# Optimization experiments

Measured on AMD Instinct MI355X. Metric: run time of the kernel, lower is better.

Reference implementation:

```python
import jax, jax.numpy as jnp
import numpy as np
import math

D_MODEL = 256
N_HEADS = 8
HEAD_DIM = D_MODEL // N_HEADS  # 32
N_LEVELS = 4
N_POINTS = 4
SHAPES = [(112, 112), (56, 56), (28, 28), (14, 14)]
LEN_IN = sum(h * w for h, w in SHAPES)  # 16660
BATCH = 1
LEN_Q = LEN_IN


def _grid_init_bias():
    # Faithful to MSDeformAttn._reset_parameters: directional grid init for sampling_offsets bias.
    thetas = np.arange(N_HEADS, dtype=np.float32) * (2.0 * math.pi / N_HEADS)
    grid = np.stack([np.cos(thetas), np.sin(thetas)], -1)
    grid = grid / np.abs(grid).max(-1, keepdims=True)
    grid = np.tile(grid[:, None, None, :], (1, N_LEVELS, N_POINTS, 1)).copy()
    for i in range(N_POINTS):
        grid[:, :, i, :] *= i + 1
    return jnp.asarray(grid.reshape(-1), dtype=jnp.float32)


def setup_inputs() -> dict:
    key = jax.random.key(0)
    ks = jax.random.split(key, 10)
    s = 1.0 / math.sqrt(D_MODEL)
    return {
        "query": jax.random.normal(ks[0], (BATCH, LEN_Q, D_MODEL), jnp.float32),
        "reference_points": jax.random.uniform(ks[1], (BATCH, LEN_Q, N_LEVELS, 2), jnp.float32),
        "input_flatten": jax.random.normal(ks[2], (BATCH, LEN_IN, D_MODEL), jnp.float32),
        "spatial_shapes": jnp.asarray(SHAPES, dtype=jnp.int32),
        "level_start_index": jnp.asarray(np.cumsum([0] + [h * w for h, w in SHAPES])[:-1], dtype=jnp.int32),
        "W_q": jax.random.normal(ks[3], (D_MODEL, D_MODEL), jnp.float32) * s,
        "b_q": jnp.zeros((D_MODEL,), jnp.float32),
        "W_k": jax.random.normal(ks[4], (D_MODEL, D_MODEL), jnp.float32) * s,
        "b_k": jnp.zeros((D_MODEL,), jnp.float32),
        "W_v": jax.random.normal(ks[5], (D_MODEL, D_MODEL), jnp.float32) * s,
        "b_v": jnp.zeros((D_MODEL,), jnp.float32),
        "W_o": jax.random.normal(ks[6], (D_MODEL, D_MODEL), jnp.float32) * s,
        "b_o": jnp.zeros((D_MODEL,), jnp.float32),
        "W_off": jax.random.normal(ks[7], (D_MODEL, N_HEADS * N_LEVELS * N_POINTS * 2), jnp.float32) * 0.01,
        "b_off": _grid_init_bias(),
    }


def _bilinear_sample(img, grid, H, W):
    # img: (B, H*W, D) flattened feature map; grid: (B, Q, P, 2) in [-1, 1] (x, y order).
    # Matches F.grid_sample(mode='bilinear', padding_mode='zeros', align_corners=False).
    B, Q, P, _ = grid.shape
    x = ((grid[..., 0] + 1.0) * W - 1.0) * 0.5
    y = ((grid[..., 1] + 1.0) * H - 1.0) * 0.5
    x0 = jnp.floor(x)
    y0 = jnp.floor(y)
    lx = x - x0
    ly = y - y0
    x0i = x0.astype(jnp.int32)
    y0i = y0.astype(jnp.int32)

    def gather(yi, xi, w):
        valid = (xi >= 0) & (xi < W) & (yi >= 0) & (yi < H)
        idx = jnp.clip(yi, 0, H - 1) * W + jnp.clip(xi, 0, W - 1)
        v = jnp.take_along_axis(img, idx.reshape(B, Q * P, 1), axis=1)
        return v.reshape(B, Q, P, -1) * (w * valid)[..., None]

    return (gather(y0i, x0i, (1.0 - ly) * (1.0 - lx))
            + gather(y0i, x0i + 1, (1.0 - ly) * lx)
            + gather(y0i + 1, x0i, ly * (1.0 - lx))
            + gather(y0i + 1, x0i + 1, ly * lx))


def reference(query, reference_points, input_flatten, spatial_shapes, level_start_index,
              W_q, b_q, W_k, b_k, W_v, b_v, W_o, b_o, W_off, b_off):
    N, Lq, C = query.shape
    M, D, L, P = N_HEADS, HEAD_DIM, N_LEVELS, N_POINTS

    q = query @ W_q + b_q                                   # (N, Lq, C)
    value = (input_flatten @ W_v + b_v).reshape(N, -1, M, D)
    key_h = (input_flatten @ W_k + b_k).reshape(N, -1, M, D)

    offsets = (q @ W_off + b_off).reshape(N, Lq, M, L, P, 2)
    # offset_normalizer = (W_l, H_l) per level
    norm = jnp.stack([spatial_shapes[:, 1], spatial_shapes[:, 0]], -1).astype(q.dtype)
    loc = reference_points[:, :, None, :, None, :] + offsets / norm[None, None, None, :, None, :]
    grids = 2.0 * loc - 1.0                                  # (N, Lq, M, L, P, 2)

    samp_v, samp_k = [], []
    start = 0
    for lid, (H, W) in enumerate(SHAPES):
        end = start + H * W
        v_l = value[:, start:end].transpose(0, 2, 1, 3).reshape(N * M, H * W, D)
        k_l = key_h[:, start:end].transpose(0, 2, 1, 3).reshape(N * M, H * W, D)
        g_l = grids[:, :, :, lid].transpose(0, 2, 1, 3, 4).reshape(N * M, Lq, P, 2)
        samp_v.append(_bilinear_sample(v_l, g_l, H, W))      # (N*M, Lq, P, D)
        samp_k.append(_bilinear_sample(k_l, g_l, H, W))
        start = end

    v_s = jnp.stack(samp_v, axis=2).reshape(N, M, Lq, L, P, D)
    k_s = jnp.stack(samp_k, axis=2).reshape(N, M, Lq, L, P, D)

    qh = q.reshape(N, Lq, M, D)
    logits = jnp.einsum('nqmd,nmqlpd->nmqlp', qh, k_s) / math.sqrt(D)
    attn = jax.nn.softmax(logits.reshape(N, M, Lq, L * P), axis=-1).reshape(N, M, Lq, L, P)

    out = jnp.einsum('nmqlp,nmqlpd->nqmd', attn, v_s).reshape(N, Lq, C)
    return out @ W_o + b_o
```

## Files before the change

### kernel.cpp

```cpp
#include <hip/hip_runtime.h>
#include <hip/hip_bf16.h>
#include <math.h>

#define LEN_IN   16660
#define D_MODEL  256
#define N_HEADS  8

typedef __attribute__((ext_vector_type(8))) short short8v;
typedef __attribute__((ext_vector_type(4))) float f32x4;
typedef _Float16 f16x2 __attribute__((ext_vector_type(2)));
typedef _Float16 f16x8 __attribute__((ext_vector_type(8)));

__device__ __forceinline__ unsigned short f2h(float f) {
  union { unsigned short u; _Float16 h; } c;
  c.h = (_Float16)f;
  return c.u;
}
__device__ __forceinline__ float h2f(unsigned short u) {
  union { unsigned short u; _Float16 h; } c;
  c.u = u;
  return (float)c.h;
}
__device__ __forceinline__ f16x2 u2h(unsigned u) {
  union { unsigned u; f16x2 h; } c;
  c.u = u;
  return c.h;
}

__global__ __launch_bounds__(256) void mega_prep(
    const float* __restrict__ inp,
    const float* __restrict__ Wq, const float* __restrict__ Wk,
    const float* __restrict__ Wv, const float* __restrict__ Woff,
    const float* __restrict__ Wo,
    const float* __restrict__ bq, const float* __restrict__ boff,
    unsigned short* __restrict__ in16,
    unsigned short* __restrict__ Btq, unsigned short* __restrict__ Btk,
    unsigned short* __restrict__ Btv, unsigned short* __restrict__ Bto,
    unsigned short* __restrict__ Btqo, float* __restrict__ bqo) {
  int b = blockIdx.x;
  int tid = threadIdx.x;

  if (b < 2048) {
    const int nq = (LEN_IN * D_MODEL) / 4;
    int i = b * 256 + tid;
    const int stride = 2048 * 256;
    for (int qd = i; qd < nq; qd += stride) {
      float4 vb = ((const float4*)inp)[qd];
      ushort4 hb = {f2h(vb.x), f2h(vb.y), f2h(vb.z), f2h(vb.w)};
      ((ushort4*)in16)[qd] = hb;
    }
    return;
  }

  if (b < 2128) {
    __shared__ float tile[64][65];
    int bb = b - 2048;
    int mat = bb >> 4, t = bb & 15;
    int ti = t >> 2, tj = t & 3;
    if (mat == 3) return;
    const float* W = (mat == 0) ? Wq : (mat == 1) ? Wk : (mat == 2) ? Wv : Wo;
    unsigned short* Bt = (mat == 0) ? Btq : (mat == 1) ? Btk : (mat == 2) ? Btv : Bto;
    #pragma unroll
    for (int i = 0; i < 16; i++) {
      int idx = tid + i * 256;
      int kr = idx >> 6, nc = idx & 63;
      tile[kr][nc] = W[(size_t)(ti * 64 + kr) * 256 + tj * 64 + nc];
    }
    __syncthreads();
    #pragma unroll
    for (int i = 0; i < 16; i++) {
      int idx = tid + i * 256;
      int nr = idx >> 6, kc = idx & 63;
      Bt[(size_t)(tj * 64 + nr) * 256 + ti * 64 + kc] = f2h(tile[kc][nr]);
    }
    return;
  }

  if (b == 2128) {
    float s = boff[tid];
    for (int i = 0; i < 256; i++) s += bq[i] * Woff[(size_t)i * 256 + tid];
    bqo[tid] = s;
    return;
  }

  {
    const int P = 40;
    __shared__ short As[64 * P], Bs[64 * P];
    int t = b - 2129;
    int m0 = (t >> 2) * 64, n0 = (t & 3) * 64;
    int w = tid >> 6, l = tid & 63;
    int r = l & 15, g = l >> 4;
    int mi = (w >> 1) * 32, ni = (w & 1) * 32;
    int sm = tid >> 2, sp = tid & 3;
    int kr = tid >> 3, nc = (tid & 7) * 8;

    f32x4 acc[2][2];
    #pragma unroll
    for (int a = 0; a < 2; a++)
      #pragma unroll
      for (int c = 0; c < 2; c++) acc[a][c] = (f32x4){0.f, 0.f, 0.f, 0.f};

    for (int k0 = 0; k0 < 256; k0 += 32) {
      const float* src = Wq + (size_t)(m0 + sm) * 256 + k0 + sp * 8;
      float4 u0 = *(const float4*)src;
      float4 u1 = *(const float4*)(src + 4);
      f16x8 hv = {(_Float16)u0.x, (_Float16)u0.y, (_Float16)u0.z, (_Float16)u0.w,
                  (_Float16)u1.x, (_Float16)u1.y, (_Float16)u1.z, (_Float16)u1.w};
      *(f16x8*)&As[sm * P + sp * 8] = hv;
      const float* wsrc = Woff + (size_t)(k0 + kr) * 256 + n0 + nc;
      float4 w0 = *(const float4*)wsrc;
      float4 w1 = *(const float4*)(wsrc + 4);
      Bs[(nc + 0) * P + kr] = (short)f2h(w0.x);
      Bs[(nc + 1) * P + kr] = (short)f2h(w0.y);
      Bs[(nc + 2) * P + kr] = (short)f2h(w0.z);
      Bs[(nc + 3) * P + kr] = (short)f2h(w0.w);
      Bs[(nc + 4) * P + kr] = (short)f2h(w1.x);
      Bs[(nc + 5) * P + kr] = (short)f2h(w1.y);
      Bs[(nc + 6) * P + kr] = (short)f2h(w1.z);
      Bs[(nc + 7) * P + kr] = (short)f2h(w1.w);
      __syncthreads();
      f16x8 af[2], bf[2];
      #pragma unroll
      for (int a = 0; a < 2; a++)
        af[a] = *(f16x8*)&As[(mi + a * 16 + r) * P + g * 8];
      #pragma unroll
      for (int c = 0; c < 2; c++)
        bf[c] = *(f16x8*)&Bs[(ni + c * 16 + r) * P + g * 8];
      #pragma unroll
      for (int a = 0; a < 2; a++)
        #pragma unroll
        for (int c = 0; c < 2; c++)
          acc[a][c] = __builtin_amdgcn_mfma_f32_16x16x32_f16(af[a], bf[c], acc[a][c], 0, 0, 0);
      __syncthreads();
    }
    #pragma unroll
    for (int a = 0; a < 2; a++)
      #pragma unroll
      for (int c = 0; c < 2; c++) {
        int col = n0 + ni + c * 16 + r;
        #pragma unroll
        for (int i = 0; i < 4; i++) {
          int row = m0 + mi + a * 16 + g * 4 + i;
          Btqo[(size_t)col * 256 + row] = f2h(acc[a][c][i]);
        }
      }
  }
}

__global__ __launch_bounds__(256) void gemm_qkv(
    const float* __restrict__ queryF, const unsigned short* __restrict__ in16,
    const unsigned short* __restrict__ Btq,
    const unsigned short* __restrict__ Btk,
    const unsigned short* __restrict__ Btv,
    const unsigned short* __restrict__ Btqo,
    const float* __restrict__ bq, const float* __restrict__ bk,
    const float* __restrict__ bv, const float* __restrict__ bqo,
    unsigned short* __restrict__ qp_out, unsigned* __restrict__ kv_out,
    unsigned short* __restrict__ offs_out, int M) {
  const int P = 72;
  __shared__ short As[128 * P], B1[64 * P], B2[64 * P];
  int z = blockIdx.z;
  const unsigned short* Bt1 = (z == 0) ? Btq : Btk;
  const unsigned short* Bt2 = (z == 0) ? Btqo : Btv;
  int tid = threadIdx.x;
  int m0 = blockIdx.x * 128, n0 = blockIdx.y * 64;
  int w = tid >> 6, l = tid & 63;
  int r = l & 15, g = l >> 4;
  int mi = (w >> 1) * 64, ni = (w & 1) * 32;
  int arow = tid >> 1, ach = (tid & 1) * 32;
  int brow = tid >> 2, bch = (tid & 3) * 16;

  f32x4 acc1[4][2], acc2[4][2];
  #pragma unroll
  for (int a = 0; a < 4; a++)
    #pragma unroll
    for (int b = 0; b < 2; b++) {
      acc1[a][b] = (f32x4){0.f, 0.f, 0.f, 0.f};
      acc2[a][b] = (f32x4){0.f, 0.f, 0.f, 0.f};
    }

  for (int k0 = 0; k0 < 256; k0 += 64) {
    int gm = m0 + arow;
    if (z == 0) {
      #pragma unroll
      for (int t = 0; t < 4; t++) {
        f16x8 hv = {0, 0, 0, 0, 0, 0, 0, 0};
        if (gm < M) {
          const float* src = queryF + (size_t)gm * 256 + k0 + ach + t * 8;
          float4 u0 = *(const float4*)src;
          float4 u1 = *(const float4*)(src + 4);
          hv = (f16x8){(_Float16)u0.x, (_Float16)u0.y, (_Float16)u0.z, (_Float16)u0.w,
                       (_Float16)u1.x, (_Float16)u1.y, (_Float16)u1.z, (_Float16)u1.w};
        }
        *(f16x8*)&As[arow * P + ach + t * 8] = hv;
      }
    } else {
      short8v a0 = {0,0,0,0,0,0,0,0}, a1 = a0, a2 = a0, a3 = a0;
      if (gm < M) {
        const unsigned short* src = in16 + (size_t)gm * 256 + k0 + ach;
        a0 = *(const short8v*)src;
        a1 = *(const short8v*)(src + 8);
        a2 = *(const short8v*)(src + 16);
        a3 = *(const short8v*)(src + 24);
      }
      *(short8v*)&As[arow * P + ach] = a0;
      *(short8v*)&As[arow * P + ach + 8] = a1;
      *(short8v*)&As[arow * P + ach + 16] = a2;
      *(short8v*)&As[arow * P + ach + 24] = a3;
    }
    {
      const unsigned short* bsrc = Bt1 + (size_t)(n0 + brow) * 256 + k0 + bch;
      *(short8v*)&B1[brow * P + bch] = *(const short8v*)bsrc;
      *(short8v*)&B1[brow * P + bch + 8] = *(const short8v*)(bsrc + 8);
      const unsigned short* bsrc2 = Bt2 + (size_t)(n0 + brow) * 256 + k0 + bch;
      *(short8v*)&B2[brow * P + bch] = *(const short8v*)bsrc2;
      *(short8v*)&B2[brow * P + bch + 8] = *(const short8v*)(bsrc2 + 8);
    }
    __syncthreads();

    f16x8 af[4][2], b1f[2][2], b2f[2][2];
    #pragma unroll
    for (int a = 0; a < 4; a++)
      #pragma unroll
      for (int ks = 0; ks < 2; ks++)
        af[a][ks] = *(f16x8*)&As[(mi + a * 16 + r) * P + ks * 32 + g * 8];
    #pragma unroll
    for (int b = 0; b < 2; b++)
      #pragma unroll
      for (int ks = 0; ks < 2; ks++) {
        b1f[b][ks] = *(f16x8*)&B1[(ni + b * 16 + r) * P + ks * 32 + g * 8];
        b2f[b][ks] = *(f16x8*)&B2[(ni + b * 16 + r) * P + ks * 32 + g * 8];
      }
    #pragma unroll
    for (int a = 0; a < 4; a++)
      #pragma unroll
      for (int b = 0; b < 2; b++)
        #pragma unroll
        for (int ks = 0; ks < 2; ks++) {
          acc1[a][b] = __builtin_amdgcn_mfma_f32_16x16x32_f16(af[a][ks], b1f[b][ks], acc1[a][b], 0, 0, 0);
          acc2[a][b] = __builtin_amdgcn_mfma_f32_16x16x32_f16(af[a][ks], b2f[b][ks], acc2[a][b], 0, 0, 0);
        }
    __syncthreads();
  }

  #pragma unroll
  for (int a = 0; a < 4; a++)
    #pragma unroll
    for (int b = 0; b < 2; b++) {
      int col = n0 + ni + b * 16 + r;
      if (z == 0) {
        float bc1 = bq[col], bc2 = bqo[col];
        #pragma unroll
        for (int i = 0; i < 4; i++) {
          int row = m0 + mi + a * 16 + g * 4 + i;
          if (row < M) {
            qp_out[(size_t)row * 256 + col] = f2h(acc1[a][b][i] + bc1);
            offs_out[(size_t)row * 256 + col] = f2h(acc2[a][b][i] + bc2);
          }
        }
      } else {
        float bkc = bk[col], bvc = bv[col];
        int hh = col >> 5, cc = col & 31;
        #pragma unroll
        for (int i = 0; i < 4; i++) {
          int row = m0 + mi + a * 16 + g * 4 + i;
          if (row < M) {
            unsigned kh = f2h(acc1[a][b][i] + bkc);
            unsigned vh = f2h(acc2[a][b][i] + bvc);
            kv_out[((size_t)hh * LEN_IN + row) * 32 + cc] = kh | (vh << 16);
          }
        }
      }
    }
}

__global__ __launch_bounds__(256) void gemm_out(
    const unsigned short* __restrict__ A,
    const unsigned short* __restrict__ Bt,
    const float* __restrict__ bias, float* __restrict__ C, int M) {
  const int P = 72;
  __shared__ short As[128 * P], Bs[64 * P];
  int tid = threadIdx.x;
  int m0 = blockIdx.x * 128, n0 = blockIdx.y * 64;
  int w = tid >> 6, l = tid & 63;
  int r = l & 15, g = l >> 4;
  int mi = (w >> 1) * 64, ni = (w & 1) * 32;
  int arow = tid >> 1, ach = (tid & 1) * 32;
  int brow = tid >> 2, bch = (tid & 3) * 16;

  f32x4 acc[4][2];
  #pragma unroll
  for (int a = 0; a < 4; a++)
    #pragma unroll
    for (int b = 0; b < 2; b++) acc[a][b] = (f32x4){0.f, 0.f, 0.f, 0.f};

  for (int k0 = 0; k0 < 256; k0 += 64) {
    int gm = m0 + arow;
    short8v a0 = {0,0,0,0,0,0,0,0}, a1 = a0, a2 = a0, a3 = a0;
    if (gm < M) {
      const unsigned short* src = A + (size_t)gm * 256 + k0 + ach;
      a0 = *(const short8v*)src;
      a1 = *(const short8v*)(src + 8);
      a2 = *(const short8v*)(src + 16);
      a3 = *(const short8v*)(src + 24);
    }
    *(short8v*)&As[arow * P + ach] = a0;
    *(short8v*)&As[arow * P + ach + 8] = a1;
    *(short8v*)&As[arow * P + ach + 16] = a2;
    *(short8v*)&As[arow * P + ach + 24] = a3;
    const unsigned short* bsrc = Bt + (size_t)(n0 + brow) * 256 + k0 + bch;
    *(short8v*)&Bs[brow * P + bch] = *(const short8v*)bsrc;
    *(short8v*)&Bs[brow * P + bch + 8] = *(const short8v*)(bsrc + 8);
    __syncthreads();

    f16x8 af[4][2], bf[2][2];
    #pragma unroll
    for (int a = 0; a < 4; a++)
      #pragma unroll
      for (int ks = 0; ks < 2; ks++)
        af[a][ks] = *(f16x8*)&As[(mi + a * 16 + r) * P + ks * 32 + g * 8];
    #pragma unroll
    for (int b = 0; b < 2; b++)
      #pragma unroll
      for (int ks = 0; ks < 2; ks++)
        bf[b][ks] = *(f16x8*)&Bs[(ni + b * 16 + r) * P + ks * 32 + g * 8];
    #pragma unroll
    for (int a = 0; a < 4; a++)
      #pragma unroll
      for (int b = 0; b < 2; b++)
        #pragma unroll
        for (int ks = 0; ks < 2; ks++)
          acc[a][b] = __builtin_amdgcn_mfma_f32_16x16x32_f16(af[a][ks], bf[b][ks], acc[a][b], 0, 0, 0);
    __syncthreads();
  }
  #pragma unroll
  for (int a = 0; a < 4; a++)
    #pragma unroll
    for (int b = 0; b < 2; b++) {
      int col = n0 + ni + b * 16 + r;
      float bc = bias[col];
      #pragma unroll
      for (int i = 0; i < 4; i++) {
        int row = m0 + mi + a * 16 + g * 4 + i;
        if (row < M) C[(size_t)row * 256 + col] = acc[a][b][i] + bc;
      }
    }
}

__global__ __launch_bounds__(256) void sample_attn(
    const unsigned short* __restrict__ qp,
    const unsigned short* __restrict__ offs,
    const float* __restrict__ rp,
    const unsigned* __restrict__ kv,
    unsigned short* __restrict__ attn_out) {
  __shared__ float vbuf[4][16][36];

  int tid = threadIdx.x;
  int wslot = tid >> 6;
  int lane = tid & 63;
  int wid = blockIdx.x * 4 + wslot;
  int q = wid >> 3;
  int h = wid & 7;

  int pt = lane >> 2;
  int c8 = (lane & 3) * 8;
  int l = pt >> 2, pp = pt & 3;
  int W = 112 >> l;
  int start = (int)((50176u - (50176u >> (2 * l))) / 3u);

  f16x2 offp = u2h(*(const unsigned*)(offs + (size_t)q * 256 + h * 32 + pt * 2));
  float2 rpp = *(const float2*)(rp + (size_t)q * 8 + l * 2);

  float x = rpp.x * (float)W + (float)offp[0] - 0.5f;
  float y = rpp.y * (float)W + (float)offp[1] - 0.5f;
  float x0f = floorf(x), y0f = floorf(y);
  float lx = x - x0f, ly = y - y0f;
  int x0 = (int)x0f, y0 = (int)y0f;
  float wx0 = 1.f - lx, wy0 = 1.f - ly;

  int Wm1 = W - 1;
  int x0c = min(max(x0, 0), Wm1), x1c = min(max(x0 + 1, 0), Wm1);
  int y0c = min(max(y0, 0), Wm1), y1c = min(max(y0 + 1, 0), Wm1);
  bool x0v = (unsigned)x0 < (unsigned)W, x1v = (unsigned)(x0 + 1) < (unsigned)W;
  bool y0v = (unsigned)y0 < (unsigned)W, y1v = (unsigned)(y0 + 1) < (unsigned)W;
  float w00 = (x0v && y0v) ? wy0 * wx0 : 0.f;
  float w01 = (x1v && y0v) ? wy0 * lx : 0.f;
  float w10 = (x0v && y1v) ? ly * wx0 : 0.f;
  float w11 = (x1v && y1v) ? ly * lx : 0.f;

  const unsigned* kvh = kv + (size_t)h * LEN_IN * 32 + c8;
  const unsigned* row0 = kvh + (size_t)(start + y0c * W) * 32;
  const unsigned* row1 = kvh + (size_t)(start + y1c * W) * 32;

  f16x2 acc[8];
  #pragma unroll
  for (int j = 0; j < 8; j++) acc[j] = (f16x2){(_Float16)0.f, (_Float16)0.f};

  const unsigned* taddr[4] = {row0 + (size_t)x0c * 32, row0 + (size_t)x1c * 32,
                              row1 + (size_t)x0c * 32, row1 + (size_t)x1c * 32};
  float twgt[4] = {w00, w01, w10, w11};
  #pragma unroll
  for (int tap = 0; tap < 4; tap++) {
    uint4 u0 = *(const uint4*)taddr[tap];
    uint4 u1 = *(const uint4*)(taddr[tap] + 4);
    _Float16 wh = (_Float16)twgt[tap];
    f16x2 w2 = {wh, wh};
    acc[0] += w2 * u2h(u0.x);
    acc[1] += w2 * u2h(u0.y);
    acc[2] += w2 * u2h(u0.z);
    acc[3] += w2 * u2h(u0.w);
    acc[4] += w2 * u2h(u1.x);
    acc[5] += w2 * u2h(u1.y);
    acc[6] += w2 * u2h(u1.z);
    acc[7] += w2 * u2h(u1.w);
  }

  uint4 qa = *(const uint4*)(qp + (size_t)q * 256 + h * 32 + c8);
  float dot = 0.f;
  f16x2 kp;
  kp[0] = acc[0][0]; kp[1] = acc[1][0];
  dot = __builtin_amdgcn_fdot2(u2h(qa.x), kp, dot, false);
  kp[0] = acc[2][0]; kp[1] = acc[3][0];
  dot = __builtin_amdgcn_fdot2(u2h(qa.y), kp, dot, false);
  kp[0] = acc[4][0]; kp[1] = acc[5][0];
  dot = __builtin_amdgcn_fdot2(u2h(qa.z), kp, dot, false);
  kp[0] = acc[6][0]; kp[1] = acc[7][0];
  dot = __builtin_amdgcn_fdot2(u2h(qa.w), kp, dot, false);
  dot += __shfl_xor(dot, 1, 64);
  dot += __shfl_xor(dot, 2, 64);

  float e = __expf(dot * 0.17677669529663687f);
  float s = e;
  s += __shfl_xor(s, 4, 64);
  s += __shfl_xor(s, 8, 64);
  s += __shfl_xor(s, 16, 64);
  s += __shfl_xor(s, 32, 64);
  float wsc = e / s;

  float4 v0 = {wsc * (float)acc[0][1], wsc * (float)acc[1][1],
               wsc * (float)acc[2][1], wsc * (float)acc[3][1]};
  float4 v1 = {wsc * (float)acc[4][1], wsc * (float)acc[5][1],
               wsc * (float)acc[6][1], wsc * (float)acc[7][1]};
  *(float4*)&vbuf[wslot][pt][c8] = v0;
  *(float4*)&vbuf[wslot][pt][c8 + 4] = v1;
  __syncthreads();

  int half = lane >> 5;
  int c = lane & 31;
  float o = 0.f;
  #pragma unroll
  for (int p = 0; p < 8; p++) o += vbuf[wslot][half * 8 + p][c];
  o += __shfl_xor(o, 32, 64);
  if (lane < 32)
    attn_out[(size_t)q * 256 + h * 32 + c] = f2h(o);
}

extern "C" void kernel_launch(void* const* d_in, const int* in_sizes, int n_in,
                              void* d_out, int out_size, void* d_ws, size_t ws_size,
                              hipStream_t stream) {
  const float* query = (const float*)d_in[0];
  const float* rp    = (const float*)d_in[1];
  const float* inp   = (const float*)d_in[2];
  const float* W_q   = (const float*)d_in[5];
  const float* b_q   = (const float*)d_in[6];
  const float* W_k   = (const float*)d_in[7];
  const float* b_k   = (const float*)d_in[8];
  const float* W_v   = (const float*)d_in[9];
  const float* b_v   = (const float*)d_in[10];
  const float* W_o   = (const float*)d_in[11];
  const float* b_o   = (const float*)d_in[12];
  const float* W_off = (const float*)d_in[13];
  const float* b_off = (const float*)d_in[14];
  float* out = (float*)d_out;

  const size_t nelem = (size_t)LEN_IN * D_MODEL;
  unsigned short* in16  = (unsigned short*)d_ws;
  unsigned short* qp    = in16 + nelem;
  unsigned short* offsb = qp + nelem;
  unsigned short* attn  = offsb + nelem;
  unsigned* kvp = (unsigned*)(attn + nelem);
  unsigned short* Btq   = (unsigned short*)(kvp + nelem);
  unsigned short* Btk   = Btq + 256 * 256;
  unsigned short* Btv   = Btk + 256 * 256;
  unsigned short* Bto   = Btv + 256 * 256;
  unsigned short* Btqo  = Bto + 256 * 256;
  float* bqo = (float*)(Btqo + 256 * 256);

  dim3 blk(256);
  dim3 ggrid((LEN_IN + 127) / 128, D_MODEL / 64);
  dim3 ggrid2((LEN_IN + 127) / 128, D_MODEL / 64, 2);

  mega_prep<<<2145, blk, 0, stream>>>(inp, W_q, W_k, W_v, W_off, W_o,
                                      b_q, b_off, in16,
                                      Btq, Btk, Btv, Bto, Btqo, bqo);

  gemm_qkv<<<ggrid2, blk, 0, stream>>>(query, in16, Btq, Btk, Btv, Btqo,
                                       b_q, b_k, b_v, bqo,
                                       qp, kvp, offsb, LEN_IN);

  int n_blocks = LEN_IN * N_HEADS / 4;
  sample_attn<<<n_blocks, blk, 0, stream>>>(qp, offsb, rp, kvp, attn);

  gemm_out<<<ggrid, blk, 0, stream>>>(attn, Bto, b_o, out, LEN_IN);
}
```

Measured before the change: 116.0 us.

## Process two query-heads per wavefront with 16-channel lanes in sampling kernel

The sampling kernel now assigns two (query, head) pairs per 64-lane wavefront, with each lane handling 16 channels of one point instead of 8. This halves the grid size and the number of lanes doing duplicated per-point coordinate and weight math, and shortens the dot-product shuffle reduction. In exchange each lane does twice the loads and accumulators, which raises register pressure and leaves fewer threads available to hide gather latency.

Result: slower. 144.1 us (+24.2%).

```diff
diff --git a/kernel.cpp b/kernel.cpp
--- a/kernel.cpp
+++ b/kernel.cpp
@@ -353,18 +353,20 @@
     const float* __restrict__ rp,
     const unsigned* __restrict__ kv,
     unsigned short* __restrict__ attn_out) {
-  __shared__ float vbuf[4][16][36];
+  __shared__ float vbuf[4][2][16][36];
 
   int tid = threadIdx.x;
   int wslot = tid >> 6;
   int lane = tid & 63;
-  int wid = blockIdx.x * 4 + wslot;
+  int qin = lane >> 5;
+  int l5 = lane & 31;
+  int pt = l5 >> 1;
+  int c16 = (l5 & 1) * 16;
+  int wid = blockIdx.x * 8 + wslot * 2 + qin;
   int q = wid >> 3;
   int h = wid & 7;
 
-  int pt = lane >> 2;
-  int c8 = (lane & 3) * 8;
-  int l = pt >> 2, pp = pt & 3;
+  int l = pt >> 2;
   int W = 112 >> l;
   int start = (int)((50176u - (50176u >> (2 * l))) / 3u);
 
@@ -388,71 +390,87 @@
   float w10 = (x0v && y1v) ? ly * wx0 : 0.f;
   float w11 = (x1v && y1v) ? ly * lx : 0.f;
 
-  const unsigned* kvh = kv + (size_t)h * LEN_IN * 32 + c8;
+  const unsigned* kvh = kv + (size_t)h * LEN_IN * 32 + c16;
   const unsigned* row0 = kvh + (size_t)(start + y0c * W) * 32;
   const unsigned* row1 = kvh + (size_t)(start + y1c * W) * 32;
-
-  f16x2 acc[8];
-  #pragma unroll
-  for (int j = 0; j < 8; j++) acc[j] = (f16x2){(_Float16)0.f, (_Float16)0.f};
-
   const unsigned* taddr[4] = {row0 + (size_t)x0c * 32, row0 + (size_t)x1c * 32,
                               row1 + (size_t)x0c * 32, row1 + (size_t)x1c * 32};
   float twgt[4] = {w00, w01, w10, w11};
+
+  f16x2 acc[16];
+  #pragma unroll
+  for (int j = 0; j < 16; j++) acc[j] = (f16x2){(_Float16)0.f, (_Float16)0.f};
+
   #pragma unroll
   for (int tap = 0; tap < 4; tap++) {
     uint4 u0 = *(const uint4*)taddr[tap];
     uint4 u1 = *(const uint4*)(taddr[tap] + 4);
+    uint4 u2 = *(const uint4*)(taddr[tap] + 8);
+    uint4 u3 = *(const uint4*)(taddr[tap] + 12);
     _Float16 wh = (_Float16)twgt[tap];
     f16x2 w2 = {wh, wh};
-    acc[0] += w2 * u2h(u0.x);
-    acc[1] += w2 * u2h(u0.y);
-    acc[2] += w2 * u2h(u0.z);
-    acc[3] += w2 * u2h(u0.w);
-    acc[4] += w2 * u2h(u1.x);
-    acc[5] += w2 * u2h(u1.y);
-    acc[6] += w2 * u2h(u1.z);
-    acc[7] += w2 * u2h(u1.w);
-  }
-
-  uint4 qa = *(const uint4*)(qp + (size_t)q * 256 + h * 32 + c8);
+    acc[0]  += w2 * u2h(u0.x);  acc[1]  += w2 * u2h(u0.y);
+    acc[2]  += w2 * u2h(u0.z);  acc[3]  += w2 * u2h(u0.w);
+    acc[4]  += w2 * u2h(u1.x);  acc[5]  += w2 * u2h(u1.y);
+    acc[6]  += w2 * u2h(u1.z);  acc[7]  += w2 * u2h(u1.w);
+    acc[8]  += w2 * u2h(u2.x);  acc[9]  += w2 * u2h(u2.y);
+    acc[10] += w2 * u2h(u2.z);  acc[11] += w2 * u2h(u2.w);
+    acc[12] += w2 * u2h(u3.x);  acc[13] += w2 * u2h(u3.y);
+    acc[14] += w2 * u2h(u3.z);  acc[15] += w2 * u2h(u3.w);
+  }
+
+  const uint4* qsrc = (const uint4*)(qp + (size_t)q * 256 + h * 32 + c16);
+  uint4 qa = qsrc[0], qb = qsrc[1];
   float dot = 0.f;
   f16x2 kp;
-  kp[0] = acc[0][0]; kp[1] = acc[1][0];
+  kp[0] = acc[0][0];  kp[1] = acc[1][0];
   dot = __builtin_amdgcn_fdot2(u2h(qa.x), kp, dot, false);
-  kp[0] = acc[2][0]; kp[1] = acc[3][0];
+  kp[0] = acc[2][0];  kp[1] = acc[3][0];
   dot = __builtin_amdgcn_fdot2(u2h(qa.y), kp, dot, false);
-  kp[0] = acc[4][0]; kp[1] = acc[5][0];
+  kp[0] = acc[4][0];  kp[1] = acc[5][0];
   dot = __builtin_amdgcn_fdot2(u2h(qa.z), kp, dot, false);
-  kp[0] = acc[6][0]; kp[1] = acc[7][0];
+  kp[0] = acc[6][0];  kp[1] = acc[7][0];
   dot = __builtin_amdgcn_fdot2(u2h(qa.w), kp, dot, false);
+  kp[0] = acc[8][0];  kp[1] = acc[9][0];
+  dot = __builtin_amdgcn_fdot2(u2h(qb.x), kp, dot, false);
+  kp[0] = acc[10][0]; kp[1] = acc[11][0];
+  dot = __builtin_amdgcn_fdot2(u2h(qb.y), kp, dot, false);
+  kp[0] = acc[12][0]; kp[1] = acc[13][0];
+  dot = __builtin_amdgcn_fdot2(u2h(qb.z), kp, dot, false);
+  kp[0] = acc[14][0]; kp[1] = acc[15][0];
+  dot = __builtin_amdgcn_fdot2(u2h(qb.w), kp, dot, false);
   dot += __shfl_xor(dot, 1, 64);
-  dot += __shfl_xor(dot, 2, 64);
 
   float e = __expf(dot * 0.17677669529663687f);
   float s = e;
+  s += __shfl_xor(s, 2, 64);
   s += __shfl_xor(s, 4, 64);
   s += __shfl_xor(s, 8, 64);
   s += __shfl_xor(s, 16, 64);
-  s += __shfl_xor(s, 32, 64);
   float wsc = e / s;
 
-  float4 v0 = {wsc * (float)acc[0][1], wsc * (float)acc[1][1],
-               wsc * (float)acc[2][1], wsc * (float)acc[3][1]};
-  float4 v1 = {wsc * (float)acc[4][1], wsc * (float)acc[5][1],
-               wsc * (float)acc[6][1], wsc * (float)acc[7][1]};
-  *(float4*)&vbuf[wslot][pt][c8] = v0;
-  *(float4*)&vbuf[wslot][pt][c8 + 4] = v1;
+  float4 o0 = {wsc * (float)acc[0][1],  wsc * (float)acc[1][1],
+               wsc * (float)acc[2][1],  wsc * (float)acc[3][1]};
+  float4 o1 = {wsc * (float)acc[4][1],  wsc * (float)acc[5][1],
+               wsc * (float)acc[6][1],  wsc * (float)acc[7][1]};
+  float4 o2 = {wsc * (float)acc[8][1],  wsc * (float)acc[9][1],
+               wsc * (float)acc[10][1], wsc * (float)acc[11][1]};
+  float4 o3 = {wsc * (float)acc[12][1], wsc * (float)acc[13][1],
+               wsc * (float)acc[14][1], wsc * (float)acc[15][1]};
+  float* vdst = &vbuf[wslot][qin][pt][c16];
+  *(float4*)(vdst + 0) = o0;
+  *(float4*)(vdst + 4) = o1;
+  *(float4*)(vdst + 8) = o2;
+  *(float4*)(vdst + 12) = o3;
   __syncthreads();
 
-  int half = lane >> 5;
+  int qo = lane >> 5;
   int c = lane & 31;
   float o = 0.f;
   #pragma unroll
-  for (int p = 0; p < 8; p++) o += vbuf[wslot][half * 8 + p][c];
-  o += __shfl_xor(o, 32, 64);
-  if (lane < 32)
-    attn_out[(size_t)q * 256 + h * 32 + c] = f2h(o);
+  for (int p = 0; p < 16; p++) o += vbuf[wslot][qo][p][c];
+  int wid2 = blockIdx.x * 8 + wslot * 2 + qo;
+  attn_out[(size_t)(wid2 >> 3) * 256 + (wid2 & 7) * 32 + c] = f2h(o);
 }
 
 extern "C" void kernel_launch(void* const* d_in, const int* in_sizes, int n_in,
@@ -498,8 +516,7 @@
                                        b_q, b_k, b_v, bqo,
                                        qp, kvp, offsb, LEN_IN);
 
-  int n_blocks = LEN_IN * N_HEADS / 4;
-  sample_attn<<<n_blocks, blk, 0, stream>>>(qp, offsb, rp, kvp, attn);
+  sample_attn<<<LEN_IN, blk, 0, stream>>>(qp, offsb, rp, kvp, attn);
 
   gemm_out<<<ggrid, blk, 0, stream>>>(attn, Bto, b_o, out, LEN_IN);
 }
```
